# Kernel optimization log

Hardware: AMD Instinct MI355X
Metric: run time of the kernel (lower is better)

## Reference

```python
import jax, jax.numpy as jnp
import numpy as np

B, T, D_IN = 32, 512, 150
D, L, H = 512, 8, 8
HD = D // H
FF = 4 * D
LLM = 512
TXT = 20


def _layernorm(x, g, b, eps=1e-5):
    m = jnp.mean(x, -1, keepdims=True)
    v = jnp.var(x, -1, keepdims=True)
    return (x - m) * jax.lax.rsqrt(v + eps) * g + b


def _timestep_pe(t, d):
    # sinusoidal PE of the diffusion step, interleaved sin/cos (torch PositionalEncoding)
    pos = t.astype(jnp.float32)[:, None]
    div = jnp.exp(-jnp.log(10000.0) * jnp.arange(0, d, 2, dtype=jnp.float32) / d)
    ang = pos * div
    return jnp.stack([jnp.sin(ang), jnp.cos(ang)], -1).reshape(t.shape[0], d)


def _rope_cos_sin(t, hd):
    inv = 1.0 / (10000.0 ** (jnp.arange(0, hd, 2, dtype=jnp.float32) / hd))
    ang = jnp.arange(t, dtype=jnp.float32)[:, None] * inv  # [T, hd/2]
    ang = jnp.concatenate([ang, ang], -1)  # [T, hd]
    return jnp.cos(ang), jnp.sin(ang)


def _apply_rope(x, cos, sin):
    # x: [B,H,T,hd]; rotate-half convention
    x1, x2 = jnp.split(x, 2, -1)
    rot = jnp.concatenate([-x2, x1], -1)
    return x * cos + rot * sin


def setup_inputs() -> dict:
    key = jax.random.key(0)
    ks = iter(jax.random.split(key, 64))
    nrm = lambda shape: jax.random.normal(next(ks), shape, jnp.float32) * 0.02
    return {
        "x": jax.random.normal(next(ks), (B, T, D_IN), jnp.float32),
        "timesteps": jax.random.randint(next(ks), (B,), 0, 1000),
        "enc_text": jax.random.normal(next(ks), (B, TXT, LLM), jnp.float32),
        "W_in": nrm((D_IN, D)), "b_in": jnp.zeros((D,), jnp.float32),
        "W_t1": nrm((D, D)), "b_t1": jnp.zeros((D,), jnp.float32),
        "W_t2": nrm((D, D)), "b_t2": jnp.zeros((D,), jnp.float32),
        "W_txt": nrm((LLM, D)), "b_txt": jnp.zeros((D,), jnp.float32),
        "ln1_g": jnp.ones((L, D), jnp.float32), "ln1_b": jnp.zeros((L, D), jnp.float32),
        "Wqkv": nrm((L, D, 3 * D)), "bqkv": jnp.zeros((L, 3 * D), jnp.float32),
        "Wo": nrm((L, D, D)), "bo": jnp.zeros((L, D), jnp.float32),
        "ln2_g": jnp.ones((L, D), jnp.float32), "ln2_b": jnp.zeros((L, D), jnp.float32),
        "W1": nrm((L, D, FF)), "b1": jnp.zeros((L, FF), jnp.float32),
        "W2": nrm((L, FF, D)), "b2": jnp.zeros((L, D), jnp.float32),
        "W_out": nrm((D, D_IN)), "b_out": jnp.zeros((D_IN,), jnp.float32),
    }


def reference(x, timesteps, enc_text, W_in, b_in, W_t1, b_t1, W_t2, b_t2,
              W_txt, b_txt, ln1_g, ln1_b, Wqkv, bqkv, Wo, bo,
              ln2_g, ln2_b, W1, b1, W2, b2, W_out, b_out):
    # conditioning fusion: timestep PE -> SiLU MLP, text mean-pool -> linear, summed
    t_emb = _timestep_pe(timesteps, D)
    t_emb = jax.nn.silu(t_emb @ W_t1 + b_t1) @ W_t2 + b_t2  # [B,D]
    txt_emb = jnp.mean(enc_text, axis=1) @ W_txt + b_txt      # [B,D]
    emb = t_emb + txt_emb
    # input process + broadcast conditioning over frames (RoPE carries positions)
    h = x @ W_in + b_in + emb[:, None, :]  # [B,T,D]
    cos, sin = _rope_cos_sin(T, HD)
    scale = 1.0 / jnp.sqrt(jnp.float32(HD))
    for i in range(L):  # 8 structurally identical pre-LN RoPE encoder blocks
        y = _layernorm(h, ln1_g[i], ln1_b[i])
        q, k, v = jnp.split(y @ Wqkv[i] + bqkv[i], 3, -1)
        q = q.reshape(B, T, H, HD).transpose(0, 2, 1, 3)
        k = k.reshape(B, T, H, HD).transpose(0, 2, 1, 3)
        v = v.reshape(B, T, H, HD).transpose(0, 2, 1, 3)
        q = _apply_rope(q, cos, sin)
        k = _apply_rope(k, cos, sin)
        attn = jax.nn.softmax(jnp.einsum('bhqd,bhkd->bhqk', q, k) * scale, -1)
        o = jnp.einsum('bhqk,bhkd->bhqd', attn, v).transpose(0, 2, 1, 3).reshape(B, T, D)
        h = h + o @ Wo[i] + bo[i]
        y = _layernorm(h, ln2_g[i], ln2_b[i])
        h = h + jax.nn.gelu(y @ W1[i] + b1[i], approximate=False) @ W2[i] + b2[i]
    return h @ W_out + b_out  # [B,T,input_feats]
```

## Files before the change

### kernel.cpp

```cpp
#include <hip/hip_runtime.h>
#include <hip/hip_bf16.h>
#include <math.h>

typedef unsigned short u16;
typedef __attribute__((ext_vector_type(8))) short bf16x8;
typedef __attribute__((ext_vector_type(4))) float f32x4;

__device__ __forceinline__ u16 f2b(float x) {
  union { float f; unsigned u; } c; c.f = x;
  unsigned r = c.u + 0x7FFFu + ((c.u >> 16) & 1u);
  return (u16)(r >> 16);
}
__device__ __forceinline__ float b2f(u16 u) {
  union { unsigned u; float f; } c; c.u = ((unsigned)u) << 16;
  return c.f;
}

__device__ __forceinline__ void gl_lds16(const u16* g, u16* l) {
  __builtin_amdgcn_global_load_lds(
      (const __attribute__((address_space(1))) void*)g,
      (__attribute__((address_space(3))) void*)l, 16, 0, 0);
}

__global__ void tconv(const float* __restrict__ W, u16* __restrict__ WT,
                      int K, int N, int KApad, int Npad) {
  __shared__ float tile[32][33];
  int z = blockIdx.z;
  W += (size_t)z * K * N;
  WT += (size_t)z * Npad * KApad;
  int n0 = blockIdx.x * 32, k0 = blockIdx.y * 32;
  int tx = threadIdx.x, ty = threadIdx.y;
  for (int i = 0; i < 4; ++i) {
    int k = k0 + ty + i * 8, n = n0 + tx;
    tile[ty + i * 8][tx] = (k < K && n < N) ? W[(size_t)k * N + n] : 0.f;
  }
  __syncthreads();
  for (int i = 0; i < 4; ++i) {
    int n = n0 + ty + i * 8, k = k0 + tx;
    WT[(size_t)n * KApad + k] = f2b(tile[tx][ty + i * 8]);
  }
}

__global__ void cond1(const int* __restrict__ ts, const float* __restrict__ Wt1,
                      const float* __restrict__ bt1, float* __restrict__ t1) {
  __shared__ float pe[512];
  int b = blockIdx.x, tid = threadIdx.x;
  float pos = (float)ts[b];
  int i2 = tid >> 1;
  float dv = expf(-0.0359778920780e0f * (float)i2);
  float ang = pos * dv;
  pe[tid] = (tid & 1) ? cosf(ang) : sinf(ang);
  __syncthreads();
  float acc = bt1[tid];
  for (int k = 0; k < 512; ++k) acc += pe[k] * Wt1[k * 512 + tid];
  t1[b * 512 + tid] = acc / (1.f + expf(-acc));
}

__global__ void cond2(const float* __restrict__ t1buf, const float* __restrict__ Wt2,
                      const float* __restrict__ bt2, const float* __restrict__ enc,
                      const float* __restrict__ Wtxt, const float* __restrict__ btxt,
                      float* __restrict__ emb) {
  __shared__ float a[512], m[512];
  int b = blockIdx.x, tid = threadIdx.x;
  a[tid] = t1buf[b * 512 + tid];
  float s = 0.f;
  for (int j = 0; j < 20; ++j) s += enc[((size_t)(b * 20 + j)) * 512 + tid];
  m[tid] = s * 0.05f;
  __syncthreads();
  float acc = bt2[tid] + btxt[tid];
  for (int k = 0; k < 512; ++k) acc += a[k] * Wt2[k * 512 + tid] + m[k] * Wtxt[k * 512 + tid];
  emb[b * 512 + tid] = acc;
}

__global__ void rope_tab(float2* __restrict__ rt) {
  int idx = blockIdx.x * 256 + threadIdx.x;
  int t = idx >> 5, i = idx & 31;
  float ang = (float)t * __expf(-0.28782313662f * (float)i);
  float sn, cn;
  sincosf(ang, &sn, &cn);
  rt[idx] = make_float2(cn, sn);
}

__global__ void xconv(const float* __restrict__ x, u16* __restrict__ xb) {
  int idx = blockIdx.x * 256 + threadIdx.x;
  int mrow = idx / 192, kk = idx - mrow * 192;
  float v = (kk < 150) ? x[(size_t)mrow * 150 + kk] : 0.f;
  xb[idx] = f2b(v);
}

__global__ __launch_bounds__(256) void ln_kernel(const float* __restrict__ h,
                                                 const float* __restrict__ g,
                                                 const float* __restrict__ be,
                                                 u16* __restrict__ y) {
  int w = threadIdx.x >> 6, lane = threadIdx.x & 63;
  int row = blockIdx.x * 4 + w;
  const float* hr = h + (size_t)row * 512 + lane * 8;
  float4 a = ((const float4*)hr)[0], b4 = ((const float4*)hr)[1];
  float s = a.x + a.y + a.z + a.w + b4.x + b4.y + b4.z + b4.w;
  float s2 = a.x * a.x + a.y * a.y + a.z * a.z + a.w * a.w +
             b4.x * b4.x + b4.y * b4.y + b4.z * b4.z + b4.w * b4.w;
#pragma unroll
  for (int o = 32; o; o >>= 1) {
    s += __shfl_xor(s, o, 64);
    s2 += __shfl_xor(s2, o, 64);
  }
  float mean = s * (1.f / 512.f);
  float var = s2 * (1.f / 512.f) - mean * mean;
  float rs = rsqrtf(var + 1e-5f);
  const float4* gp = (const float4*)(g + lane * 8);
  const float4* bp = (const float4*)(be + lane * 8);
  float4 g0 = gp[0], g1 = gp[1], be0 = bp[0], be1 = bp[1];
  ushort4 o0, o1;
  o0.x = f2b((a.x - mean) * rs * g0.x + be0.x);
  o0.y = f2b((a.y - mean) * rs * g0.y + be0.y);
  o0.z = f2b((a.z - mean) * rs * g0.z + be0.z);
  o0.w = f2b((a.w - mean) * rs * g0.w + be0.w);
  o1.x = f2b((b4.x - mean) * rs * g1.x + be1.x);
  o1.y = f2b((b4.y - mean) * rs * g1.y + be1.y);
  o1.z = f2b((b4.z - mean) * rs * g1.z + be1.z);
  o1.w = f2b((b4.w - mean) * rs * g1.w + be1.w);
  ushort4* yp = (ushort4*)(y + (size_t)row * 512 + lane * 8);
  yp[0] = o0;
  yp[1] = o1;
}

__global__ __launch_bounds__(256) void attn_mfma2(const u16* __restrict__ qk,
                                                  const u16* __restrict__ vt,
                                                  u16* __restrict__ o) {
  __shared__ u16 Qs[64 * 64];
  __shared__ u16 KVs[128 * 64];
  __shared__ u16 Ps[64 * 128];
  const int tid = threadIdx.x;
  const int qt = blockIdx.x, h = blockIdx.y, b = blockIdx.z;
  const int lane = tid & 63, w = tid >> 6;
  const int q = lane >> 4, c16 = lane & 15;

  const size_t qbase = (size_t)(b * 512 + qt * 64) * 1024 + h * 64;
  {
    int row0 = tid >> 3, cs = tid & 7;
#pragma unroll
    for (int rep = 0; rep < 2; ++rep) {
      int r2 = rep * 32 + row0;
      int g = cs ^ (r2 & 7);
      gl_lds16(qk + qbase + (size_t)r2 * 1024 + g * 8, Qs + rep * 2048 + tid * 8);
    }
  }

  f32x4 o_acc[4];
  float m_st[4], l_st[4];
#pragma unroll
  for (int jd = 0; jd < 4; ++jd) o_acc[jd] = (f32x4){0.f, 0.f, 0.f, 0.f};
#pragma unroll
  for (int r = 0; r < 4; ++r) { m_st[r] = -1e30f; l_st[r] = 0.f; }

  const size_t kbase = (size_t)b * 512 * 1024 + 512 + h * 64;
  const size_t vtbase = ((size_t)(b * 8 + h) * 64) * 512;

  for (int kt = 0; kt < 4; ++kt) {
    if (kt) __syncthreads();
    {
      int row0 = tid >> 3, cs = tid & 7;
#pragma unroll
      for (int rep = 0; rep < 4; ++rep) {
        int r2 = rep * 32 + row0;
        int g = cs ^ (r2 & 7);
        gl_lds16(qk + kbase + (size_t)(kt * 128 + r2) * 1024 + g * 8,
                 KVs + rep * 2048 + tid * 8);
      }
    }
    __syncthreads();

    f32x4 s_acc[8];
#pragma unroll
    for (int j = 0; j < 8; ++j) s_acc[j] = (f32x4){0.f, 0.f, 0.f, 0.f};
#pragma unroll
    for (int ka = 0; ka < 2; ++ka) {
      bf16x8 af, bf[8];
      {
        int row = w * 16 + c16;
        af = *(const bf16x8*)(Qs + row * 64 + (((ka * 4 + q) ^ (row & 7)) * 8));
      }
#pragma unroll
      for (int j = 0; j < 8; ++j) {
        int row = j * 16 + c16;
        bf[j] = *(const bf16x8*)(KVs + row * 64 + (((ka * 4 + q) ^ (row & 7)) * 8));
      }
#pragma unroll
      for (int j = 0; j < 8; ++j)
        s_acc[j] = __builtin_amdgcn_mfma_f32_16x16x32_bf16(af, bf[j], s_acc[j], 0, 0, 0);
    }
    __syncthreads();

    {
      int vr0 = tid >> 4, cc = tid & 15;
#pragma unroll
      for (int rep = 0; rep < 4; ++rep) {
        int row = rep * 16 + vr0;
        int g2 = cc ^ (row & 15);
        gl_lds16(vt + vtbase + (size_t)row * 512 + kt * 128 + g2 * 8,
                 KVs + rep * 2048 + tid * 8);
      }
    }

#pragma unroll
    for (int r = 0; r < 4; ++r) {
      float mx = s_acc[0][r];
#pragma unroll
      for (int j = 1; j < 8; ++j) mx = fmaxf(mx, s_acc[j][r]);
      mx = fmaxf(mx, __shfl_xor(mx, 1, 64));
      mx = fmaxf(mx, __shfl_xor(mx, 2, 64));
      mx = fmaxf(mx, __shfl_xor(mx, 4, 64));
      mx = fmaxf(mx, __shfl_xor(mx, 8, 64));
      float mn = fmaxf(m_st[r], mx);
      float al = __expf(m_st[r] - mn);
      m_st[r] = mn;
      float sum = 0.f;
#pragma unroll
      for (int j = 0; j < 8; ++j) {
        float p = __expf(s_acc[j][r] - mn);
        s_acc[j][r] = p;
        sum += p;
      }
      sum += __shfl_xor(sum, 1, 64);
      sum += __shfl_xor(sum, 2, 64);
      sum += __shfl_xor(sum, 4, 64);
      sum += __shfl_xor(sum, 8, 64);
      l_st[r] = l_st[r] * al + sum;
#pragma unroll
      for (int jd = 0; jd < 4; ++jd) o_acc[jd][r] *= al;
    }

#pragma unroll
    for (int j = 0; j < 8; ++j)
#pragma unroll
      for (int r = 0; r < 4; ++r) {
        int prow = w * 16 + q * 4 + r;
        int col = j * 16 + c16;
        int cp = col >> 3;
        Ps[prow * 128 + ((cp ^ (prow & 15)) * 8) + (col & 7)] = f2b(s_acc[j][r]);
      }
    __syncthreads();

#pragma unroll
    for (int s = 0; s < 4; ++s) {
      bf16x8 af, bv[4];
      {
        int row = w * 16 + c16;
        af = *(const bf16x8*)(Ps + row * 128 + (((s * 4 + q) ^ (row & 15)) * 8));
      }
#pragma unroll
      for (int jd = 0; jd < 4; ++jd) {
        int row = jd * 16 + c16;
        bv[jd] = *(const bf16x8*)(KVs + row * 128 + (((s * 4 + q) ^ (row & 15)) * 8));
      }
#pragma unroll
      for (int jd = 0; jd < 4; ++jd)
        o_acc[jd] = __builtin_amdgcn_mfma_f32_16x16x32_bf16(af, bv[jd], o_acc[jd], 0, 0, 0);
    }
  }

#pragma unroll
  for (int r = 0; r < 4; ++r) {
    float inv = 1.f / l_st[r];
    int trow = qt * 64 + w * 16 + q * 4 + r;
#pragma unroll
    for (int jd = 0; jd < 4; ++jd)
      o[(size_t)(b * 512 + trow) * 512 + h * 64 + jd * 16 + c16] = f2b(o_acc[jd][r] * inv);
  }
}

template <int MODE>
__global__ __launch_bounds__(256) void gemm_bf16(
    const u16* __restrict__ A, const u16* __restrict__ BT,
    const float* __restrict__ bias, const float* aux, void* aux2, void* Cout,
    int KA, int ldc, int nx) {
  __shared__ u16 As[128 * 64];
  __shared__ u16 Bs[128 * 64];
  const int tid = threadIdx.x;
  int bid = blockIdx.x;
  int rr = bid & 7, gg = bid >> 3;
  int xN = gg % nx, yM = rr + 8 * (gg / nx);
  const int tileN = xN * 128;
  const int tileM = yM * 128;
  const int lane = tid & 63, w = tid >> 6;
  const int mw = (w >> 1) * 64, nw = (w & 1) * 64;
  const int q = lane >> 4, c16 = lane & 15;

  f32x4 acc[4][4];
#pragma unroll
  for (int i = 0; i < 4; ++i)
#pragma unroll
    for (int j = 0; j < 4; ++j) acc[i][j] = (f32x4){0.f, 0.f, 0.f, 0.f};

  const int rowA0 = tid >> 3;
  const int cs = tid & 7;
  const int KT = KA >> 6;
  for (int kt = 0; kt < KT; ++kt) {
    __syncthreads();
#pragma unroll
    for (int rep = 0; rep < 4; ++rep) {
      int row = rep * 32 + rowA0;
      int g = cs ^ (row & 7);
      gl_lds16(A + (size_t)(tileM + row) * KA + kt * 64 + g * 8,
               (u16*)((char*)As + rep * 4096 + tid * 16));
    }
#pragma unroll
    for (int rep = 0; rep < 4; ++rep) {
      int row = rep * 32 + rowA0;
      int g = cs ^ (row & 7);
      gl_lds16(BT + (size_t)(tileN + row) * KA + kt * 64 + g * 8,
               (u16*)((char*)Bs + rep * 4096 + tid * 16));
    }
    __syncthreads();
#pragma unroll
    for (int ks = 0; ks < 2; ++ks) {
      bf16x8 af[4], bfr[4];
#pragma unroll
      for (int i = 0; i < 4; ++i) {
        int m = mw + i * 16 + c16;
        int ca = (ks * 4 + q) ^ (m & 7);
        af[i] = *(const bf16x8*)((const char*)As + m * 128 + ca * 16);
        int n = nw + i * 16 + c16;
        int cb = (ks * 4 + q) ^ (n & 7);
        bfr[i] = *(const bf16x8*)((const char*)Bs + n * 128 + cb * 16);
      }
#pragma unroll
      for (int i = 0; i < 4; ++i)
#pragma unroll
        for (int j = 0; j < 4; ++j)
          acc[i][j] = __builtin_amdgcn_mfma_f32_16x16x32_bf16(af[i], bfr[j], acc[i][j], 0, 0, 0);
    }
  }

  if (MODE == 5) {
    const float2* rt = (const float2*)aux;
    u16* qk = (u16*)Cout;
    u16* vtp = (u16*)aux2;
#pragma unroll
    for (int i = 0; i < 4; ++i) {
      int row = tileM + mw + i * 16 + q * 4;
      int bb = row >> 9, t0 = row & 511;
#pragma unroll
      for (int jp = 0; jp < 2; ++jp) {
        int colA = tileN + nw + jp * 16 + c16;
        if (colA < 1024) {
          int colB = colA + 32;
          int d31 = colA & 31;
          float scl = (colA < 512) ? 0.125f : 1.f;
          float bA = bias[colA], bB = bias[colB];
#pragma unroll
          for (int r = 0; r < 4; ++r) {
            float2 cs2 = rt[(t0 + r) * 32 + d31];
            float x1 = acc[i][jp][r] + bA;
            float x2 = acc[i][jp + 2][r] + bB;
            size_t rbase = (size_t)(row + r) * 1024;
            qk[rbase + colA] = f2b((x1 * cs2.x - x2 * cs2.y) * scl);
            qk[rbase + colB] = f2b((x2 * cs2.x + x1 * cs2.y) * scl);
          }
        } else {
#pragma unroll
          for (int jj = jp; jj < 4; jj += 2) {
            int col = tileN + nw + jj * 16 + c16;
            int hh = (col - 1024) >> 6, d = col & 63;
            float bv2 = bias[col];
            ushort4 pk;
            pk.x = f2b(acc[i][jj][0] + bv2);
            pk.y = f2b(acc[i][jj][1] + bv2);
            pk.z = f2b(acc[i][jj][2] + bv2);
            pk.w = f2b(acc[i][jj][3] + bv2);
            *(ushort4*)(vtp + ((size_t)((bb * 8 + hh) * 64 + d)) * 512 + t0) = pk;
          }
        }
      }
    }
    return;
  }

#pragma unroll
  for (int i = 0; i < 4; ++i) {
#pragma unroll
    for (int j = 0; j < 4; ++j) {
      int col = tileN + nw + j * 16 + c16;
      float bv = (MODE == 4) ? 0.f : bias[col];
#pragma unroll
      for (int r = 0; r < 4; ++r) {
        int row = tileM + mw + i * 16 + q * 4 + r;
        float v = acc[i][j][r] + bv;
        if (MODE == 0) {
          ((float*)Cout)[(size_t)row * ldc + col] = v + aux[(row >> 9) * 512 + col];
        } else if (MODE == 2) {
          size_t idx = (size_t)row * ldc + col;
          ((float*)Cout)[idx] = aux[idx] + v;
        } else if (MODE == 3) {
          float u = v * v;
          float p = __builtin_fmaf(0.044715f, u, 1.0f);
          float t2 = v * p;
          float e = __expf(-1.59576912f * t2);
          float r2 = __builtin_amdgcn_rcpf(1.0f + e);
          ((u16*)Cout)[(size_t)row * ldc + col] = f2b(v * r2);
        } else if (MODE == 4) {
          if (col < 150) ((float*)Cout)[(size_t)row * 150 + col] = acc[i][j][r] + bias[col];
        } else if (MODE == 6) {
          size_t idx = (size_t)row * ldc + col;
          float v2 = aux[idx] + v;
          ((float*)Cout)[idx] = v2;
          ((u16*)aux2)[idx] = f2b(v2);
        }
      }
    }
  }
}

extern "C" void kernel_launch(void* const* d_in, const int* in_sizes, int n_in,
                              void* d_out, int out_size, void* d_ws, size_t ws_size,
                              hipStream_t stream) {
  const float* x = (const float*)d_in[0];
  const int* tsteps = (const int*)d_in[1];
  const float* enc = (const float*)d_in[2];
  const float* W_in = (const float*)d_in[3];
  const float* b_in = (const float*)d_in[4];
  const float* W_t1 = (const float*)d_in[5];
  const float* b_t1 = (const float*)d_in[6];
  const float* W_t2 = (const float*)d_in[7];
  const float* b_t2 = (const float*)d_in[8];
  const float* W_txt = (const float*)d_in[9];
  const float* b_txt = (const float*)d_in[10];
  const float* ln1_g = (const float*)d_in[11];
  const float* ln1_b = (const float*)d_in[12];
  const float* Wqkv = (const float*)d_in[13];
  const float* bqkv = (const float*)d_in[14];
  const float* Wo = (const float*)d_in[15];
  const float* bo = (const float*)d_in[16];
  const float* ln2_g = (const float*)d_in[17];
  const float* ln2_b = (const float*)d_in[18];
  const float* W1 = (const float*)d_in[19];
  const float* b1 = (const float*)d_in[20];
  const float* W2 = (const float*)d_in[21];
  const float* b2 = (const float*)d_in[22];
  const float* W_out = (const float*)d_in[23];
  const float* b_out = (const float*)d_in[24];

  char* ws = (char*)d_ws;
  u16* WT_in = (u16*)(ws + 0);
  u16* WT_qkv = (u16*)(ws + 196608);
  u16* WT_o = (u16*)(ws + 12779520);
  u16* WT_1 = (u16*)(ws + 16973824);
  u16* WT_2 = (u16*)(ws + 33751040);
  u16* WT_out = (u16*)(ws + 50528256);
  u16* xb = (u16*)(ws + 50790400);
  float* hf = (float*)(ws + 57081856);
  u16* yb = (u16*)(ws + 90636288);
  u16* qkvb = (u16*)(ws + 107413504);
  float2* rtab = (float2*)(ws + 107413504 + 33554432);
  u16* ob = (u16*)(ws + 157745152);
  u16* ffb = (u16*)(ws + 174522368);
  u16* hb = (u16*)(ws + 241631232);
  u16* vtb = hb;
  float* embf = (float*)(ws + 258408448);
  float* t1c = (float*)(ws + 258473984);

  dim3 tb(32, 8);
  tconv<<<dim3(16, 6, 1), tb, 0, stream>>>(W_in, WT_in, 150, 512, 192, 512);
  tconv<<<dim3(48, 16, 8), tb, 0, stream>>>(Wqkv, WT_qkv, 512, 1536, 512, 1536);
  tconv<<<dim3(16, 16, 8), tb, 0, stream>>>(Wo, WT_o, 512, 512, 512, 512);
  tconv<<<dim3(64, 16, 8), tb, 0, stream>>>(W1, WT_1, 512, 2048, 512, 2048);
  tconv<<<dim3(16, 64, 8), tb, 0, stream>>>(W2, WT_2, 2048, 512, 2048, 512);
  tconv<<<dim3(8, 16, 1), tb, 0, stream>>>(W_out, WT_out, 512, 150, 512, 256);

  cond1<<<32, 512, 0, stream>>>(tsteps, W_t1, b_t1, t1c);
  cond2<<<32, 512, 0, stream>>>(t1c, W_t2, b_t2, enc, W_txt, b_txt, embf);
  rope_tab<<<64, 256, 0, stream>>>(rtab);
  xconv<<<12288, 256, 0, stream>>>(x, xb);

  gemm_bf16<0><<<4 * 128, 256, 0, stream>>>(xb, WT_in, b_in, embf, nullptr, hf, 192, 512, 4);

  for (int l = 0; l < 8; ++l) {
    ln_kernel<<<4096, 256, 0, stream>>>(hf, ln1_g + l * 512, ln1_b + l * 512, yb);
    gemm_bf16<5><<<12 * 128, 256, 0, stream>>>(yb, WT_qkv + (size_t)l * 1536 * 512,
                                               bqkv + l * 1536, (const float*)rtab,
                                               vtb, qkvb, 512, 1024, 12);
    attn_mfma2<<<dim3(8, 8, 32), 256, 0, stream>>>(qkvb, vtb, ob);
    gemm_bf16<2><<<4 * 128, 256, 0, stream>>>(ob, WT_o + (size_t)l * 512 * 512,
                                              bo + l * 512, hf, nullptr, hf, 512, 512, 4);
    ln_kernel<<<4096, 256, 0, stream>>>(hf, ln2_g + l * 512, ln2_b + l * 512, yb);
    gemm_bf16<3><<<16 * 128, 256, 0, stream>>>(yb, WT_1 + (size_t)l * 2048 * 512,
                                               b1 + l * 2048, nullptr, nullptr, ffb, 512, 2048, 16);
    if (l < 7) {
      gemm_bf16<2><<<4 * 128, 256, 0, stream>>>(ffb, WT_2 + (size_t)l * 512 * 2048,
                                                b2 + l * 512, hf, nullptr, hf, 2048, 512, 4);
    } else {
      gemm_bf16<6><<<4 * 128, 256, 0, stream>>>(ffb, WT_2 + (size_t)l * 512 * 2048,
                                                b2 + l * 512, hf, hb, hf, 2048, 512, 4);
    }
  }

  gemm_bf16<4><<<2 * 128, 256, 0, stream>>>(hb, WT_out, b_out, nullptr, nullptr, d_out, 512, 150, 2);
}
```

Measured before the change: 2.342 ms.

## Split-K the Wo and W2 residual GEMMs with atomic accumulation into h

Adds a SPLITK template parameter and a new epilogue mode that atomically adds partial products into the fp32 residual stream. The Wo GEMM is split 2-way and the W2 GEMM 4-way along K, which multiplies the block count from 512 to 1024 and 2048 to fill the device better. The final bf16 copy of h moves into a separate conversion kernel. The cost is fp32 atomic traffic to the residual, and the summation order is no longer deterministic.

```diff
diff --git a/kernel.cpp b/kernel.cpp
--- a/kernel.cpp
+++ b/kernel.cpp
@@ -86,6 +86,18 @@
   int mrow = idx / 192, kk = idx - mrow * 192;
   float v = (kk < 150) ? x[(size_t)mrow * 150 + kk] : 0.f;
   xb[idx] = f2b(v);
+}
+
+__global__ __launch_bounds__(256) void h2b(const float* __restrict__ hf,
+                                           u16* __restrict__ hb) {
+  int idx = (blockIdx.x * 256 + threadIdx.x) * 8;
+  float4 a = *(const float4*)(hf + idx);
+  float4 b = *(const float4*)(hf + idx + 4);
+  ushort4 o0, o1;
+  o0.x = f2b(a.x); o0.y = f2b(a.y); o0.z = f2b(a.z); o0.w = f2b(a.w);
+  o1.x = f2b(b.x); o1.y = f2b(b.y); o1.z = f2b(b.z); o1.w = f2b(b.w);
+  *(ushort4*)(hb + idx) = o0;
+  *(ushort4*)(hb + idx + 4) = o1;
 }
 
 __global__ __launch_bounds__(256) void ln_kernel(const float* __restrict__ h,
@@ -269,7 +281,7 @@
   }
 }
 
-template <int MODE>
+template <int MODE, int SPLITK = 1>
 __global__ __launch_bounds__(256) void gemm_bf16(
     const u16* __restrict__ A, const u16* __restrict__ BT,
     const float* __restrict__ bias, const float* aux, void* aux2, void* Cout,
@@ -278,6 +290,12 @@
   __shared__ u16 Bs[128 * 64];
   const int tid = threadIdx.x;
   int bid = blockIdx.x;
+  int chunk = 0;
+  if (SPLITK > 1) {
+    int nin = nx * 128;
+    chunk = bid / nin;
+    bid -= chunk * nin;
+  }
   int rr = bid & 7, gg = bid >> 3;
   int xN = gg % nx, yM = rr + 8 * (gg / nx);
   const int tileN = xN * 128;
@@ -294,8 +312,9 @@
 
   const int rowA0 = tid >> 3;
   const int cs = tid & 7;
-  const int KT = KA >> 6;
-  for (int kt = 0; kt < KT; ++kt) {
+  const int KT = (KA >> 6) / SPLITK;
+  const int kt0 = chunk * KT;
+  for (int kt = kt0; kt < kt0 + KT; ++kt) {
     __syncthreads();
 #pragma unroll
     for (int rep = 0; rep < 4; ++rep) {
@@ -381,7 +400,8 @@
 #pragma unroll
     for (int j = 0; j < 4; ++j) {
       int col = tileN + nw + j * 16 + c16;
-      float bv = (MODE == 4) ? 0.f : bias[col];
+      float bv = (MODE == 4) ? 0.f
+                             : ((MODE == 7 && chunk != 0) ? 0.f : bias[col]);
 #pragma unroll
       for (int r = 0; r < 4; ++r) {
         int row = tileM + mw + i * 16 + q * 4 + r;
@@ -405,6 +425,9 @@
           float v2 = aux[idx] + v;
           ((float*)Cout)[idx] = v2;
           ((u16*)aux2)[idx] = f2b(v2);
+        } else if (MODE == 7) {
+          size_t idx = (size_t)row * ldc + col;
+          unsafeAtomicAdd(&((float*)Cout)[idx], v);
         }
       }
     }
@@ -480,19 +503,17 @@
                                                bqkv + l * 1536, (const float*)rtab,
                                                vtb, qkvb, 512, 1024, 12);
     attn_mfma2<<<dim3(8, 8, 32), 256, 0, stream>>>(qkvb, vtb, ob);
-    gemm_bf16<2><<<4 * 128, 256, 0, stream>>>(ob, WT_o + (size_t)l * 512 * 512,
-                                              bo + l * 512, hf, nullptr, hf, 512, 512, 4);
+    gemm_bf16<7, 2><<<2 * 4 * 128, 256, 0, stream>>>(ob, WT_o + (size_t)l * 512 * 512,
+                                                     bo + l * 512, nullptr, nullptr, hf,
+                                                     512, 512, 4);
     ln_kernel<<<4096, 256, 0, stream>>>(hf, ln2_g + l * 512, ln2_b + l * 512, yb);
     gemm_bf16<3><<<16 * 128, 256, 0, stream>>>(yb, WT_1 + (size_t)l * 2048 * 512,
                                                b1 + l * 2048, nullptr, nullptr, ffb, 512, 2048, 16);
-    if (l < 7) {
-      gemm_bf16<2><<<4 * 128, 256, 0, stream>>>(ffb, WT_2 + (size_t)l * 512 * 2048,
-                                                b2 + l * 512, hf, nullptr, hf, 2048, 512, 4);
-    } else {
-      gemm_bf16<6><<<4 * 128, 256, 0, stream>>>(ffb, WT_2 + (size_t)l * 512 * 2048,
-                                                b2 + l * 512, hf, hb, hf, 2048, 512, 4);
-    }
-  }
-
+    gemm_bf16<7, 4><<<4 * 4 * 128, 256, 0, stream>>>(ffb, WT_2 + (size_t)l * 512 * 2048,
+                                                     b2 + l * 512, nullptr, nullptr, hf,
+                                                     2048, 512, 4);
+  }
+
+  h2b<<<4096, 256, 0, stream>>>(hf, hb);
   gemm_bf16<4><<<2 * 128, 256, 0, stream>>>(hb, WT_out, b_out, nullptr, nullptr, d_out, 512, 150, 2);
 }
```

After: 3.136 ms. +33.9%, slower.
